# Kernel tuning notes

Measured on AMD Instinct MI355X. Metric: run time of the kernel, lower is better.

The kernel has to match this reference:

```python
import jax, jax.numpy as jnp
import numpy as np

N_HEADS = 32
N_KV_HEADS = 8
HEAD_DIM = 64
ROPE_THETA = 10000.0
NEG_INF = -1e9


def apply_rope(t, offset=0):
    # t: [B, H, L, hd]; half-split (rotate-half) RoPE convention
    B, H, L, hd = t.shape
    pos = jnp.arange(offset, offset + L, dtype=jnp.float32)            # [L]
    inv_freq = 1.0 / (ROPE_THETA ** (jnp.arange(0, hd, 2, dtype=jnp.float32) / hd))  # [hd/2]
    ang = pos[:, None] * inv_freq[None, :]                              # [L, hd/2]
    cos = jnp.cos(ang).astype(t.dtype)
    sin = jnp.sin(ang).astype(t.dtype)
    t1, t2 = jnp.split(t, 2, axis=-1)                                   # each [B,H,L,hd/2]
    return jnp.concatenate([t1 * cos - t2 * sin, t1 * sin + t2 * cos], axis=-1)


def setup_inputs() -> dict:
    key = jax.random.key(0)
    ks = jax.random.split(key, 6)
    B, L, D = 1, 2048, 2048
    x = jax.random.normal(ks[0], (B, L, D), dtype=jnp.float32)
    attn_scale = jnp.ones((1,), dtype=jnp.float32)
    # causal additive mask: 0 on/below diagonal, -1e9 above
    mask = jnp.where(jnp.tril(jnp.ones((L, L), dtype=bool)), 0.0, NEG_INF).astype(jnp.float32)
    s = 0.02
    Wq = jax.random.normal(ks[1], (N_HEADS * HEAD_DIM, D), dtype=jnp.float32) * s
    Wk = jax.random.normal(ks[2], (N_KV_HEADS * HEAD_DIM, D), dtype=jnp.float32) * s
    Wv = jax.random.normal(ks[3], (N_KV_HEADS * HEAD_DIM, D), dtype=jnp.float32) * s
    Wo = jax.random.normal(ks[4], (D, N_HEADS * HEAD_DIM), dtype=jnp.float32) * s
    return {"x": x, "attn_scale": attn_scale, "mask": mask,
            "Wq": Wq, "Wk": Wk, "Wv": Wv, "Wo": Wo}


def reference(x, attn_scale, mask, Wq, Wk, Wv, Wo):
    B, L, D = x.shape
    scale = HEAD_DIM ** -0.5
    # projections (nn.Linear: y = x @ W.T)
    q = (x @ Wq.T).reshape(B, L, N_HEADS, HEAD_DIM).transpose(0, 2, 1, 3)     # [B,H,L,hd]
    k = (x @ Wk.T).reshape(B, L, N_KV_HEADS, HEAD_DIM).transpose(0, 2, 1, 3)  # [B,Hk,L,hd]
    v = (x @ Wv.T).reshape(B, L, N_KV_HEADS, HEAD_DIM).transpose(0, 2, 1, 3)
    q = apply_rope(q)
    k = apply_rope(k)
    q = q * attn_scale  # elementwise attn_scale applied to queries
    # GQA: repeat kv heads
    rep = N_HEADS // N_KV_HEADS
    k = jnp.repeat(k, rep, axis=1)
    v = jnp.repeat(v, rep, axis=1)
    scores = jnp.einsum('bhld,bhmd->bhlm', q, k) * scale + mask
    probs = jax.nn.softmax(scores, axis=-1)
    out = jnp.einsum('bhlm,bhmd->bhld', probs, v)          # [B,H,L,hd]
    out = out.transpose(0, 2, 1, 3).reshape(B, L, N_HEADS * HEAD_DIM)
    return out @ Wo.T
```

## Files before the change

### kernel.cpp

```cpp
#include <hip/hip_runtime.h>
#include <stdint.h>

typedef short bf16x8 __attribute__((ext_vector_type(8)));
typedef float f32x4 __attribute__((ext_vector_type(4)));

__device__ __forceinline__ unsigned short f2bf(float f) {
  uint32_t u = __float_as_uint(f);
  u = (u + 0x7FFFu + ((u >> 16) & 1u)) >> 16;
  return (unsigned short)u;
}
__device__ __forceinline__ float bf2f(unsigned short h) {
  return __uint_as_float(((uint32_t)h) << 16);
}

__device__ __forceinline__ void gload16(const void* g, void* lds) {
  const __attribute__((address_space(1))) char* gp =
      (const __attribute__((address_space(1))) char*)(uintptr_t)g;
  __attribute__((address_space(3))) char* sp =
      (__attribute__((address_space(3))) char*)(uint32_t)(uintptr_t)lds;
  __builtin_amdgcn_global_load_lds(gp, sp, 16, 0, 0);
}

__global__ void k_cvt_all(const float* __restrict__ x, const float* __restrict__ Wq,
                          const float* __restrict__ Wk, const float* __restrict__ Wv,
                          const float* __restrict__ Wo, unsigned short* __restrict__ xb,
                          unsigned short* __restrict__ Wcat, unsigned short* __restrict__ Wob) {
  int b = blockIdx.x;
  const float* src;
  unsigned short* dst;
  int off;
  if (b < 4096)       { src = x;  dst = xb;                  off = b; }
  else if (b < 8192)  { src = Wq; dst = Wcat;                off = b - 4096; }
  else if (b < 9216)  { src = Wk; dst = Wcat + 2048 * 2048;  off = b - 8192; }
  else if (b < 10240) { src = Wv; dst = Wcat + 2560 * 2048;  off = b - 9216; }
  else                { src = Wo; dst = Wob;                  off = b - 10240; }
  int i = off * 256 + threadIdx.x;
  float4 v = ((const float4*)src)[i];
  ushort4 o;
  o.x = f2bf(v.x); o.y = f2bf(v.y); o.z = f2bf(v.z); o.w = f2bf(v.w);
  ((ushort4*)dst)[i] = o;
}

template <int OUTF32>
__global__ __launch_bounds__(256) void k_gemm(const unsigned short* __restrict__ A,
                                              const unsigned short* __restrict__ B,
                                              void* __restrict__ Cout,
                                              int M, int N, int K) {
  __shared__ unsigned short As[2][128 * 64];
  __shared__ unsigned short Bs[2][128 * 64];
  const int tid = threadIdx.x;
  const int w = tid >> 6, lane = tid & 63;
  const int g = lane >> 4, cl = lane & 15;
  const int nTn = N >> 7;
  const int per = gridDim.x >> 3;
  const int bid = (blockIdx.x & 7) * per + (blockIdx.x >> 3);
  const int tm = bid / nTn, tn = bid % nTn;
  const int m0 = tm << 7, n0 = tn << 7;
  const int wm = (w >> 1) << 6, wn = (w & 1) << 6;
  f32x4 acc[4][4] = {};

  auto stage = [&](int kt, int b) {
#pragma unroll
    for (int it = 0; it < 8; ++it) {
      int cc = tid + it * 256;
      int half = cc >> 10;
      int c3 = cc & 1023;
      int row = c3 >> 3, kb = (c3 & 7) << 4;
      const unsigned short* base = half ? (B + (size_t)(n0 + row) * K + kt)
                                        : (A + (size_t)(m0 + row) * K + kt);
      const char* src = (const char*)base + (kb ^ ((row & 7) << 4));
      char* dstl = (char*)(half ? Bs[b] : As[b]) + c3 * 16;
      gload16(src, dstl);
    }
  };

  stage(0, 0);
  asm volatile("s_waitcnt vmcnt(0)" ::: "memory");
  __syncthreads();
  int buf = 0;

  for (int kt = 0; kt < K; kt += 64) {
    if (kt + 64 < K) stage(kt + 64, buf ^ 1);
#pragma unroll
    for (int ks = 0; ks < 2; ++ks) {
      bf16x8 af[4], bfr[4];
#pragma unroll
      for (int i = 0; i < 4; ++i) {
        int row = wm + i * 16 + cl;
        int kb = ((g << 4) + (ks << 6)) ^ ((row & 7) << 4);
        af[i] = *(const bf16x8*)((const char*)As[buf] + row * 128 + kb);
      }
#pragma unroll
      for (int j = 0; j < 4; ++j) {
        int row = wn + j * 16 + cl;
        int kb = ((g << 4) + (ks << 6)) ^ ((row & 7) << 4);
        bfr[j] = *(const bf16x8*)((const char*)Bs[buf] + row * 128 + kb);
      }
#pragma unroll
      for (int i = 0; i < 4; ++i)
#pragma unroll
        for (int j = 0; j < 4; ++j)
          acc[i][j] = __builtin_amdgcn_mfma_f32_16x16x32_bf16(af[i], bfr[j], acc[i][j], 0, 0, 0);
    }
    asm volatile("s_waitcnt vmcnt(0)" ::: "memory");
    __syncthreads();
    buf ^= 1;
  }
#pragma unroll
  for (int i = 0; i < 4; ++i)
#pragma unroll
    for (int j = 0; j < 4; ++j)
#pragma unroll
      for (int r = 0; r < 4; ++r) {
        int row = m0 + wm + i * 16 + (g << 2) + r;
        int col = n0 + wn + j * 16 + cl;
        float v = acc[i][j][r];
        if (OUTF32)
          ((float*)Cout)[(size_t)row * N + col] = v;
        else
          ((unsigned short*)Cout)[(size_t)row * N + col] = f2bf(v);
      }
}

__global__ void k_ropevt(unsigned short* __restrict__ qkv, const float* __restrict__ scale_p,
                         unsigned short* __restrict__ vt) {
  __shared__ unsigned short tl[64][80];
  if (blockIdx.x < 2560) {
    int idx = blockIdx.x * 256 + threadIdx.x;
    int l = idx / 320;
    int u = idx - l * 320;
    int h = u >> 3;
    int i4 = (u & 7) << 2;
    int colbase = (h < 32) ? (h << 6) : (2048 + ((h - 32) << 6));
    unsigned short* p = qkv + (size_t)l * 3072 + colbase + i4;
    float sc = (h < 32) ? (scale_p[0] * 0.125f * 1.4426950408889634f) : 1.0f;
    ushort4 a = *(const ushort4*)p;
    ushort4 b = *(const ushort4*)(p + 32);
    unsigned short av[4] = {a.x, a.y, a.z, a.w};
    unsigned short bv[4] = {b.x, b.y, b.z, b.w};
    unsigned short r1[4], r2[4];
#pragma unroll
    for (int j = 0; j < 4; ++j) {
      int i = i4 + j;
      float invf = __expf(-(float)i * 0.2878231366242557f);
      float ang = (float)l * invf;
      float cs = cosf(ang), sn = sinf(ang);
      float x1 = bf2f(av[j]), x2 = bf2f(bv[j]);
      r1[j] = f2bf((x1 * cs - x2 * sn) * sc);
      r2[j] = f2bf((x1 * sn + x2 * cs) * sc);
    }
    ushort4 oa = {r1[0], r1[1], r1[2], r1[3]};
    ushort4 ob = {r2[0], r2[1], r2[2], r2[3]};
    *(ushort4*)p = oa;
    *(ushort4*)(p + 32) = ob;
  } else {
    const int tid = threadIdx.x;
    const int bb = blockIdx.x - 2560;
    const int hk = bb >> 5, lt = bb & 31;
    const int l0 = lt << 6;
#pragma unroll
    for (int it = 0; it < 2; ++it) {
      int cc = tid + it * 256;
      int lr = cc >> 3, d0 = (cc & 7) << 3;
      uint4 v = *(const uint4*)(qkv + (size_t)(l0 + lr) * 3072 + 2560 + hk * 64 + d0);
      *(uint4*)&tl[lr][d0] = v;
    }
    __syncthreads();
#pragma unroll
    for (int it = 0; it < 2; ++it) {
      int cc = tid + it * 256;
      int dr = cc >> 3, le = (cc & 7) << 3;
      unsigned short tmp[8] __attribute__((aligned(16)));
#pragma unroll
      for (int j = 0; j < 8; ++j) tmp[j] = tl[le + j][dr];
      *(uint4*)(vt + (size_t)(hk * 64 + dr) * 2048 + l0 + le) = *(const uint4*)tmp;
    }
  }
}

__global__ __launch_bounds__(256) void k_attn(const unsigned short* __restrict__ qkv,
                                              const unsigned short* __restrict__ vt,
                                              unsigned short* __restrict__ ao) {
  __shared__ unsigned short Ks[2][64 * 64];
  __shared__ unsigned short Vs[3][64 * 64];
  __shared__ unsigned short Ps[4 * 16 * 64];
  const int tid = threadIdx.x;
  const int w = tid >> 6, lane = tid & 63;
  const int g = lane >> 4, cl = lane & 15;
  const int h = blockIdx.x & 31;
  const int qb = 31 - (blockIdx.x >> 5);
  const int q0 = qb << 6;
  const int hk = h >> 2;
  const int qg = q0 + w * 16 + cl;

  const unsigned short* qptr = qkv + (size_t)qg * 3072 + h * 64 + g * 8;
  bf16x8 qf0 = *(const bf16x8*)qptr;
  bf16x8 qf1 = *(const bf16x8*)(qptr + 32);

  float m_run = -3e38f, l_run = 0.0f;
  f32x4 acc[4] = {};

  const unsigned short* kbase = qkv + 2048 + hk * 64;
  const unsigned short* vbase = vt + (size_t)hk * 64 * 2048;
  char* myP = (char*)Ps + w * 2048;

  auto stageK = [&](int ck, int b) {
    const int kv0 = ck << 6;
#pragma unroll
    for (int it = 0; it < 2; ++it) {
      int cc = tid + it * 256;
      int row = cc >> 3, kb = (cc & 7) << 4;
      const char* src = (const char*)(kbase + (size_t)(kv0 + row) * 3072) + (kb ^ ((row & 7) << 4));
      gload16(src, (char*)Ks[b] + cc * 16);
    }
  };
  auto stageV = [&](int ck, int b) {
    const int kv0 = ck << 6;
#pragma unroll
    for (int it = 0; it < 2; ++it) {
      int cc = tid + it * 256;
      int row = cc >> 3, kb = (cc & 7) << 4;
      const char* src = (const char*)(vbase + (size_t)row * 2048 + kv0) + (kb ^ ((row & 7) << 4));
      gload16(src, (char*)Vs[b] + cc * 16);
    }
  };

  stageK(0, 0); stageV(0, 0);
  if (qb >= 1) { stageK(1, 1); stageV(1, 1); }
  asm volatile("s_waitcnt vmcnt(0)" ::: "memory");
  __syncthreads();

  float svP[4][4];
  {
    const char* Kc = (const char*)Ks[0];
    __builtin_amdgcn_s_setprio(1);
#pragma unroll
    for (int t = 0; t < 4; ++t) {
      f32x4 st = {};
#pragma unroll
      for (int ks = 0; ks < 2; ++ks) {
        int row = t * 16 + cl;
        int kb = ((g << 4) + (ks << 6)) ^ ((row & 7) << 4);
        bf16x8 kf = *(const bf16x8*)(Kc + row * 128 + kb);
        st = __builtin_amdgcn_mfma_f32_16x16x32_bf16(kf, ks ? qf1 : qf0, st, 0, 0, 0);
      }
#pragma unroll
      for (int r = 0; r < 4; ++r) svP[t][r] = st[r];
    }
    __builtin_amdgcn_s_setprio(0);
  }
  __syncthreads();

  for (int i = 0; i <= qb; ++i) {
    const bool deep = (i + 2 <= qb);
    if (deep) stageK(i + 2, (i + 2) & 1);

    float svN[4][4];
    if (i < qb) {
      const char* Kc = (const char*)Ks[(i + 1) & 1];
      __builtin_amdgcn_s_setprio(1);
#pragma unroll
      for (int t = 0; t < 4; ++t) {
        f32x4 st = {};
#pragma unroll
        for (int ks = 0; ks < 2; ++ks) {
          int row = t * 16 + cl;
          int kb = ((g << 4) + (ks << 6)) ^ ((row & 7) << 4);
          bf16x8 kf = *(const bf16x8*)(Kc + row * 128 + kb);
          st = __builtin_amdgcn_mfma_f32_16x16x32_bf16(kf, ks ? qf1 : qf0, st, 0, 0, 0);
        }
#pragma unroll
        for (int r = 0; r < 4; ++r) svN[t][r] = st[r];
      }
      __builtin_amdgcn_s_setprio(0);
    }

    if (deep) stageV(i + 2, (i + 2) % 3);

    if (i == qb) {
      const int kv0 = i << 6;
#pragma unroll
      for (int t = 0; t < 4; ++t)
#pragma unroll
        for (int r = 0; r < 4; ++r) {
          int kvg = kv0 + t * 16 + (g << 2) + r;
          if (kvg > qg) svP[t][r] = -1e9f;
        }
    }
    float pm[4];
#pragma unroll
    for (int t = 0; t < 4; ++t)
      pm[t] = fmaxf(fmaxf(svP[t][0], svP[t][1]), fmaxf(svP[t][2], svP[t][3]));
    float pmax = fmaxf(fmaxf(pm[0], pm[1]), fmaxf(pm[2], pm[3]));
    pmax = fmaxf(pmax, __shfl_xor(pmax, 16));
    pmax = fmaxf(pmax, __shfl_xor(pmax, 32));
    if (!__all(pmax - m_run <= 8.0f)) {
      float m_new = fmaxf(m_run, pmax);
      float fac = __builtin_exp2f(m_run - m_new);
      float fr[4];
#pragma unroll
      for (int r = 0; r < 4; ++r) fr[r] = __shfl(fac, (g << 2) + r);
#pragma unroll
      for (int t = 0; t < 4; ++t) {
        acc[t][0] *= fr[0]; acc[t][1] *= fr[1]; acc[t][2] *= fr[2]; acc[t][3] *= fr[3];
      }
      l_run *= fac;
      m_run = m_new;
    }
    float ps[4];
#pragma unroll
    for (int t = 0; t < 4; ++t) {
      float e0 = __builtin_exp2f(svP[t][0] - m_run);
      float e1 = __builtin_exp2f(svP[t][1] - m_run);
      float e2 = __builtin_exp2f(svP[t][2] - m_run);
      float e3 = __builtin_exp2f(svP[t][3] - m_run);
      ps[t] = (e0 + e1) + (e2 + e3);
      uint32_t d0, d1;
      asm("v_cvt_pk_bf16_f32 %0, %1, %2" : "=v"(d0) : "v"(e0), "v"(e1));
      asm("v_cvt_pk_bf16_f32 %0, %1, %2" : "=v"(d1) : "v"(e2), "v"(e3));
      uint2 dd; dd.x = d0; dd.y = d1;
      int kb = ((t << 5) + (g << 3)) ^ ((cl & 7) << 4);
      *(uint2*)(myP + cl * 128 + kb) = dd;
    }
    float psum = (ps[0] + ps[1]) + (ps[2] + ps[3]);
    psum += __shfl_xor(psum, 16);
    psum += __shfl_xor(psum, 32);
    l_run += psum;

    {
      const char* Vc = (const char*)Vs[i % 3];
      __builtin_amdgcn_s_setprio(1);
#pragma unroll
      for (int ks = 0; ks < 2; ++ks) {
        int kbp = ((g << 4) + (ks << 6)) ^ ((cl & 7) << 4);
        bf16x8 pf = *(const bf16x8*)(myP + cl * 128 + kbp);
#pragma unroll
        for (int t = 0; t < 4; ++t) {
          int row = t * 16 + cl;
          int kbv = ((g << 4) + (ks << 6)) ^ ((row & 7) << 4);
          bf16x8 vf = *(const bf16x8*)(Vc + row * 128 + kbv);
          acc[t] = __builtin_amdgcn_mfma_f32_16x16x32_bf16(pf, vf, acc[t], 0, 0, 0);
        }
      }
      __builtin_amdgcn_s_setprio(0);
    }

    if (i < qb) {
      if (deep)
        asm volatile("s_waitcnt vmcnt(2)" ::: "memory");
      else
        asm volatile("s_waitcnt vmcnt(0)" ::: "memory");
      __syncthreads();
#pragma unroll
      for (int t = 0; t < 4; ++t)
#pragma unroll
        for (int r = 0; r < 4; ++r) svP[t][r] = svN[t][r];
    }
  }

  float li[4];
#pragma unroll
  for (int r = 0; r < 4; ++r) li[r] = 1.0f / __shfl(l_run, (g << 2) + r);
#pragma unroll
  for (int t = 0; t < 4; ++t)
#pragma unroll
    for (int r = 0; r < 4; ++r) {
      int row = q0 + w * 16 + (g << 2) + r;
      int col = h * 64 + t * 16 + cl;
      ao[(size_t)row * 2048 + col] = f2bf(acc[t][r] * li[r]);
    }
}

extern "C" void kernel_launch(void* const* d_in, const int* in_sizes, int n_in,
                              void* d_out, int out_size, void* d_ws, size_t ws_size,
                              hipStream_t stream) {
  (void)in_sizes; (void)n_in; (void)out_size; (void)ws_size;
  const float* x  = (const float*)d_in[0];
  const float* sc = (const float*)d_in[1];
  const float* Wq = (const float*)d_in[3];
  const float* Wk = (const float*)d_in[4];
  const float* Wv = (const float*)d_in[5];
  const float* Wo = (const float*)d_in[6];
  float* out = (float*)d_out;
  char* ws = (char*)d_ws;
  unsigned short* xb   = (unsigned short*)(ws);
  unsigned short* Wcat = (unsigned short*)(ws + 8388608);
  unsigned short* Wob  = (unsigned short*)(ws + 20971520);
  unsigned short* QKV  = (unsigned short*)(ws + 29360128);
  unsigned short* VT   = (unsigned short*)(ws + 41943040);
  unsigned short* AO   = (unsigned short*)(ws + 44040192);

  k_cvt_all<<<14336, 256, 0, stream>>>(x, Wq, Wk, Wv, Wo, xb, Wcat, Wob);
  k_gemm<0><<<384, 256, 0, stream>>>(xb, Wcat, QKV, 2048, 3072, 2048);
  k_ropevt<<<2816, 256, 0, stream>>>(QKV, sc, VT);
  k_attn<<<1024, 256, 0, stream>>>(QKV, VT, AO);
  k_gemm<1><<<256, 256, 0, stream>>>(AO, Wob, out, 2048, 2048, 2048);
}
```

Before: 128.9 us.

## Split attention into single-wave blocks with V loaded directly to registers

The attention kernel changes from 256-thread blocks, where four waves share staged K and V tiles, to 64-thread single-wave blocks, each handling 16 query rows, with four times as many blocks. V fragments are now read straight from global memory into registers instead of through a triple-buffered LDS stage. K is single-buffered in LDS with a prefetch of the next chunk, and the block barriers are removed. This gives up K/V reuse across four waves and the deep software pipeline in exchange for no barriers and more scheduling freedom. Global K/V traffic roughly quadruples, and memory latency is less well hidden.

```diff
diff --git a/kernel.cpp b/kernel.cpp
--- a/kernel.cpp
+++ b/kernel.cpp
@@ -178,61 +178,58 @@
   }
 }
 
-__global__ __launch_bounds__(256) void k_attn(const unsigned short* __restrict__ qkv,
-                                              const unsigned short* __restrict__ vt,
-                                              unsigned short* __restrict__ ao) {
-  __shared__ unsigned short Ks[2][64 * 64];
-  __shared__ unsigned short Vs[3][64 * 64];
-  __shared__ unsigned short Ps[4 * 16 * 64];
-  const int tid = threadIdx.x;
-  const int w = tid >> 6, lane = tid & 63;
+__global__ __launch_bounds__(64, 4) void k_attn(const unsigned short* __restrict__ qkv,
+                                                const unsigned short* __restrict__ vt,
+                                                unsigned short* __restrict__ ao) {
+  __shared__ unsigned short Ks[64 * 64];
+  __shared__ unsigned short Ps[16 * 64];
+  const int lane = threadIdx.x;
   const int g = lane >> 4, cl = lane & 15;
   const int h = blockIdx.x & 31;
-  const int qb = 31 - (blockIdx.x >> 5);
-  const int q0 = qb << 6;
+  const int rest = blockIdx.x >> 5;
+  const int qb = 31 - (rest >> 2);
+  const int quarter = rest & 3;
+  const int q0 = (qb << 6) + (quarter << 4);
   const int hk = h >> 2;
-  const int qg = q0 + w * 16 + cl;
+  const int qg = q0 + cl;
 
   const unsigned short* qptr = qkv + (size_t)qg * 3072 + h * 64 + g * 8;
+  const unsigned short* kbase = qkv + 2048 + hk * 64;
+  const unsigned short* vbase = vt + (size_t)hk * 64 * 2048;
+  char* myP = (char*)Ps;
+
+  auto stageK = [&](int ck) {
+    const int kv0 = ck << 6;
+#pragma unroll
+    for (int it = 0; it < 8; ++it) {
+      int cc = lane + it * 64;
+      int row = cc >> 3, kb = (cc & 7) << 4;
+      const char* src = (const char*)(kbase + (size_t)(kv0 + row) * 3072) + (kb ^ ((row & 7) << 4));
+      gload16(src, (char*)Ks + cc * 16);
+    }
+  };
+
+  stageK(0);
   bf16x8 qf0 = *(const bf16x8*)qptr;
   bf16x8 qf1 = *(const bf16x8*)(qptr + 32);
+  asm volatile("s_waitcnt vmcnt(0)" ::: "memory");
 
   float m_run = -3e38f, l_run = 0.0f;
   f32x4 acc[4] = {};
 
-  const unsigned short* kbase = qkv + 2048 + hk * 64;
-  const unsigned short* vbase = vt + (size_t)hk * 64 * 2048;
-  char* myP = (char*)Ps + w * 2048;
-
-  auto stageK = [&](int ck, int b) {
-    const int kv0 = ck << 6;
-#pragma unroll
-    for (int it = 0; it < 2; ++it) {
-      int cc = tid + it * 256;
-      int row = cc >> 3, kb = (cc & 7) << 4;
-      const char* src = (const char*)(kbase + (size_t)(kv0 + row) * 3072) + (kb ^ ((row & 7) << 4));
-      gload16(src, (char*)Ks[b] + cc * 16);
-    }
-  };
-  auto stageV = [&](int ck, int b) {
-    const int kv0 = ck << 6;
-#pragma unroll
-    for (int it = 0; it < 2; ++it) {
-      int cc = tid + it * 256;
-      int row = cc >> 3, kb = (cc & 7) << 4;
-      const char* src = (const char*)(vbase + (size_t)row * 2048 + kv0) + (kb ^ ((row & 7) << 4));
-      gload16(src, (char*)Vs[b] + cc * 16);
-    }
-  };
-
-  stageK(0, 0); stageV(0, 0);
-  if (qb >= 1) { stageK(1, 1); stageV(1, 1); }
-  asm volatile("s_waitcnt vmcnt(0)" ::: "memory");
-  __syncthreads();
-
-  float svP[4][4];
-  {
-    const char* Kc = (const char*)Ks[0];
+  for (int i = 0; i <= qb; ++i) {
+    const int kv0 = i << 6;
+
+    bf16x8 vfr[2][4];
+#pragma unroll
+    for (int ks = 0; ks < 2; ++ks)
+#pragma unroll
+      for (int t = 0; t < 4; ++t)
+        vfr[ks][t] = *(const bf16x8*)(vbase + (size_t)(t * 16 + cl) * 2048 + kv0 + ks * 32 + g * 8);
+
+    asm volatile("s_waitcnt vmcnt(8)" ::: "memory");
+
+    float svP[4][4];
     __builtin_amdgcn_s_setprio(1);
 #pragma unroll
     for (int t = 0; t < 4; ++t) {
@@ -241,44 +238,18 @@
       for (int ks = 0; ks < 2; ++ks) {
         int row = t * 16 + cl;
         int kb = ((g << 4) + (ks << 6)) ^ ((row & 7) << 4);
-        bf16x8 kf = *(const bf16x8*)(Kc + row * 128 + kb);
+        bf16x8 kf = *(const bf16x8*)((const char*)Ks + row * 128 + kb);
         st = __builtin_amdgcn_mfma_f32_16x16x32_bf16(kf, ks ? qf1 : qf0, st, 0, 0, 0);
       }
 #pragma unroll
       for (int r = 0; r < 4; ++r) svP[t][r] = st[r];
     }
     __builtin_amdgcn_s_setprio(0);
-  }
-  __syncthreads();
-
-  for (int i = 0; i <= qb; ++i) {
-    const bool deep = (i + 2 <= qb);
-    if (deep) stageK(i + 2, (i + 2) & 1);
-
-    float svN[4][4];
-    if (i < qb) {
-      const char* Kc = (const char*)Ks[(i + 1) & 1];
-      __builtin_amdgcn_s_setprio(1);
-#pragma unroll
-      for (int t = 0; t < 4; ++t) {
-        f32x4 st = {};
-#pragma unroll
-        for (int ks = 0; ks < 2; ++ks) {
-          int row = t * 16 + cl;
-          int kb = ((g << 4) + (ks << 6)) ^ ((row & 7) << 4);
-          bf16x8 kf = *(const bf16x8*)(Kc + row * 128 + kb);
-          st = __builtin_amdgcn_mfma_f32_16x16x32_bf16(kf, ks ? qf1 : qf0, st, 0, 0, 0);
-        }
-#pragma unroll
-        for (int r = 0; r < 4; ++r) svN[t][r] = st[r];
-      }
-      __builtin_amdgcn_s_setprio(0);
-    }
-
-    if (deep) stageV(i + 2, (i + 2) % 3);
+
+    asm volatile("s_waitcnt lgkmcnt(0)" ::: "memory");
+    if (i < qb) stageK(i + 1);
 
     if (i == qb) {
-      const int kv0 = i << 6;
 #pragma unroll
       for (int t = 0; t < 4; ++t)
 #pragma unroll
@@ -327,35 +298,16 @@
     psum += __shfl_xor(psum, 32);
     l_run += psum;
 
-    {
-      const char* Vc = (const char*)Vs[i % 3];
-      __builtin_amdgcn_s_setprio(1);
-#pragma unroll
-      for (int ks = 0; ks < 2; ++ks) {
-        int kbp = ((g << 4) + (ks << 6)) ^ ((cl & 7) << 4);
-        bf16x8 pf = *(const bf16x8*)(myP + cl * 128 + kbp);
-#pragma unroll
-        for (int t = 0; t < 4; ++t) {
-          int row = t * 16 + cl;
-          int kbv = ((g << 4) + (ks << 6)) ^ ((row & 7) << 4);
-          bf16x8 vf = *(const bf16x8*)(Vc + row * 128 + kbv);
-          acc[t] = __builtin_amdgcn_mfma_f32_16x16x32_bf16(pf, vf, acc[t], 0, 0, 0);
-        }
-      }
-      __builtin_amdgcn_s_setprio(0);
-    }
-
-    if (i < qb) {
-      if (deep)
-        asm volatile("s_waitcnt vmcnt(2)" ::: "memory");
-      else
-        asm volatile("s_waitcnt vmcnt(0)" ::: "memory");
-      __syncthreads();
+    __builtin_amdgcn_s_setprio(1);
+#pragma unroll
+    for (int ks = 0; ks < 2; ++ks) {
+      int kbp = ((g << 4) + (ks << 6)) ^ ((cl & 7) << 4);
+      bf16x8 pf = *(const bf16x8*)(myP + cl * 128 + kbp);
 #pragma unroll
       for (int t = 0; t < 4; ++t)
-#pragma unroll
-        for (int r = 0; r < 4; ++r) svP[t][r] = svN[t][r];
-    }
+        acc[t] = __builtin_amdgcn_mfma_f32_16x16x32_bf16(pf, vfr[ks][t], acc[t], 0, 0, 0);
+    }
+    __builtin_amdgcn_s_setprio(0);
   }
 
   float li[4];
@@ -365,7 +317,7 @@
   for (int t = 0; t < 4; ++t)
 #pragma unroll
     for (int r = 0; r < 4; ++r) {
-      int row = q0 + w * 16 + (g << 2) + r;
+      int row = q0 + (g << 2) + r;
       int col = h * 64 + t * 16 + cl;
       ao[(size_t)row * 2048 + col] = f2bf(acc[t][r] * li[r]);
     }
@@ -393,6 +345,6 @@
   k_cvt_all<<<14336, 256, 0, stream>>>(x, Wq, Wk, Wv, Wo, xb, Wcat, Wob);
   k_gemm<0><<<384, 256, 0, stream>>>(xb, Wcat, QKV, 2048, 3072, 2048);
   k_ropevt<<<2816, 256, 0, stream>>>(QKV, sc, VT);
-  k_attn<<<1024, 256, 0, stream>>>(QKV, VT, AO);
+  k_attn<<<4096, 64, 0, stream>>>(QKV, VT, AO);
   k_gemm<1><<<256, 256, 0, stream>>>(AO, Wob, out, 2048, 2048, 2048);
 }
```

Result: slower. 218.4 us (+69.4%).

## Fuse RoPE and scaling into QKV GEMM epilogue; simplify attention V buffering

Applied to the files above, without the earlier changes.

RoPE rotation and the query scale move into the QKV projection GEMM epilogue, operating on fp32 accumulators before the bf16 store. This removes a separate read-modify-write pass over Q and K and leaves a small kernel that only transposes V. The attention kernel also goes from triple- to double-buffered V staging, with V prefetched one tile ahead and a full vmcnt(0) wait each iteration. That cuts LDS use but may expose more load latency. Rotating before bf16 rounding also slightly changes numerics.

```diff
diff --git a/kernel.cpp b/kernel.cpp
--- a/kernel.cpp
+++ b/kernel.cpp
@@ -41,11 +41,12 @@
   ((ushort4*)dst)[i] = o;
 }
 
-template <int OUTF32>
+template <int OUTF32, int ROPE>
 __global__ __launch_bounds__(256) void k_gemm(const unsigned short* __restrict__ A,
                                               const unsigned short* __restrict__ B,
                                               void* __restrict__ Cout,
-                                              int M, int N, int K) {
+                                              int M, int N, int K,
+                                              const float* __restrict__ scale_p) {
   __shared__ unsigned short As[2][128 * 64];
   __shared__ unsigned short Bs[2][128 * 64];
   const int tid = threadIdx.x;
@@ -106,6 +107,31 @@
     __syncthreads();
     buf ^= 1;
   }
+
+  if (ROPE && n0 < 2560) {
+    float s0v = scale_p[0] * 0.125f * 1.4426950408889634f;
+    float sc = (n0 < 2048) ? s0v : 1.0f;
+    float invf[2];
+#pragma unroll
+    for (int j = 0; j < 2; ++j)
+      invf[j] = __expf(-(float)(j * 16 + cl) * 0.2878231366242557f);
+#pragma unroll
+    for (int i = 0; i < 4; ++i)
+#pragma unroll
+      for (int r = 0; r < 4; ++r) {
+        float pos = (float)(m0 + wm + i * 16 + (g << 2) + r);
+#pragma unroll
+        for (int j = 0; j < 2; ++j) {
+          float ang = pos * invf[j];
+          float sn, cs;
+          __sincosf(ang, &sn, &cs);
+          float t1 = acc[i][j][r], t2 = acc[i][j + 2][r];
+          acc[i][j][r] = (t1 * cs - t2 * sn) * sc;
+          acc[i][j + 2][r] = (t1 * sn + t2 * cs) * sc;
+        }
+      }
+  }
+
 #pragma unroll
   for (int i = 0; i < 4; ++i)
 #pragma unroll
@@ -122,59 +148,27 @@
       }
 }
 
-__global__ void k_ropevt(unsigned short* __restrict__ qkv, const float* __restrict__ scale_p,
-                         unsigned short* __restrict__ vt) {
+__global__ void k_vt(const unsigned short* __restrict__ qkv, unsigned short* __restrict__ vt) {
   __shared__ unsigned short tl[64][80];
-  if (blockIdx.x < 2560) {
-    int idx = blockIdx.x * 256 + threadIdx.x;
-    int l = idx / 320;
-    int u = idx - l * 320;
-    int h = u >> 3;
-    int i4 = (u & 7) << 2;
-    int colbase = (h < 32) ? (h << 6) : (2048 + ((h - 32) << 6));
-    unsigned short* p = qkv + (size_t)l * 3072 + colbase + i4;
-    float sc = (h < 32) ? (scale_p[0] * 0.125f * 1.4426950408889634f) : 1.0f;
-    ushort4 a = *(const ushort4*)p;
-    ushort4 b = *(const ushort4*)(p + 32);
-    unsigned short av[4] = {a.x, a.y, a.z, a.w};
-    unsigned short bv[4] = {b.x, b.y, b.z, b.w};
-    unsigned short r1[4], r2[4];
-#pragma unroll
-    for (int j = 0; j < 4; ++j) {
-      int i = i4 + j;
-      float invf = __expf(-(float)i * 0.2878231366242557f);
-      float ang = (float)l * invf;
-      float cs = cosf(ang), sn = sinf(ang);
-      float x1 = bf2f(av[j]), x2 = bf2f(bv[j]);
-      r1[j] = f2bf((x1 * cs - x2 * sn) * sc);
-      r2[j] = f2bf((x1 * sn + x2 * cs) * sc);
-    }
-    ushort4 oa = {r1[0], r1[1], r1[2], r1[3]};
-    ushort4 ob = {r2[0], r2[1], r2[2], r2[3]};
-    *(ushort4*)p = oa;
-    *(ushort4*)(p + 32) = ob;
-  } else {
-    const int tid = threadIdx.x;
-    const int bb = blockIdx.x - 2560;
-    const int hk = bb >> 5, lt = bb & 31;
-    const int l0 = lt << 6;
-#pragma unroll
-    for (int it = 0; it < 2; ++it) {
-      int cc = tid + it * 256;
-      int lr = cc >> 3, d0 = (cc & 7) << 3;
-      uint4 v = *(const uint4*)(qkv + (size_t)(l0 + lr) * 3072 + 2560 + hk * 64 + d0);
-      *(uint4*)&tl[lr][d0] = v;
-    }
-    __syncthreads();
-#pragma unroll
-    for (int it = 0; it < 2; ++it) {
-      int cc = tid + it * 256;
-      int dr = cc >> 3, le = (cc & 7) << 3;
-      unsigned short tmp[8] __attribute__((aligned(16)));
-#pragma unroll
-      for (int j = 0; j < 8; ++j) tmp[j] = tl[le + j][dr];
-      *(uint4*)(vt + (size_t)(hk * 64 + dr) * 2048 + l0 + le) = *(const uint4*)tmp;
-    }
+  const int tid = threadIdx.x;
+  const int hk = blockIdx.x >> 5, lt = blockIdx.x & 31;
+  const int l0 = lt << 6;
+#pragma unroll
+  for (int it = 0; it < 2; ++it) {
+    int cc = tid + it * 256;
+    int lr = cc >> 3, d0 = (cc & 7) << 3;
+    uint4 v = *(const uint4*)(qkv + (size_t)(l0 + lr) * 3072 + 2560 + hk * 64 + d0);
+    *(uint4*)&tl[lr][d0] = v;
+  }
+  __syncthreads();
+#pragma unroll
+  for (int it = 0; it < 2; ++it) {
+    int cc = tid + it * 256;
+    int dr = cc >> 3, le = (cc & 7) << 3;
+    unsigned short tmp[8] __attribute__((aligned(16)));
+#pragma unroll
+    for (int j = 0; j < 8; ++j) tmp[j] = tl[le + j][dr];
+    *(uint4*)(vt + (size_t)(hk * 64 + dr) * 2048 + l0 + le) = *(const uint4*)tmp;
   }
 }
 
@@ -182,7 +176,7 @@
                                               const unsigned short* __restrict__ vt,
                                               unsigned short* __restrict__ ao) {
   __shared__ unsigned short Ks[2][64 * 64];
-  __shared__ unsigned short Vs[3][64 * 64];
+  __shared__ unsigned short Vs[2][64 * 64];
   __shared__ unsigned short Ps[4 * 16 * 64];
   const int tid = threadIdx.x;
   const int w = tid >> 6, lane = tid & 63;
@@ -226,7 +220,7 @@
   };
 
   stageK(0, 0); stageV(0, 0);
-  if (qb >= 1) { stageK(1, 1); stageV(1, 1); }
+  if (qb >= 1) stageK(1, 1);
   asm volatile("s_waitcnt vmcnt(0)" ::: "memory");
   __syncthreads();
 
@@ -252,8 +246,8 @@
   __syncthreads();
 
   for (int i = 0; i <= qb; ++i) {
-    const bool deep = (i + 2 <= qb);
-    if (deep) stageK(i + 2, (i + 2) & 1);
+    if (i + 2 <= qb) stageK(i + 2, i & 1);
+    if (i + 1 <= qb) stageV(i + 1, (i + 1) & 1);
 
     float svN[4][4];
     if (i < qb) {
@@ -274,8 +268,6 @@
       }
       __builtin_amdgcn_s_setprio(0);
     }
-
-    if (deep) stageV(i + 2, (i + 2) % 3);
 
     if (i == qb) {
       const int kv0 = i << 6;
@@ -328,7 +320,7 @@
     l_run += psum;
 
     {
-      const char* Vc = (const char*)Vs[i % 3];
+      const char* Vc = (const char*)Vs[i & 1];
       __builtin_amdgcn_s_setprio(1);
 #pragma unroll
       for (int ks = 0; ks < 2; ++ks) {
@@ -346,10 +338,7 @@
     }
 
     if (i < qb) {
-      if (deep)
-        asm volatile("s_waitcnt vmcnt(2)" ::: "memory");
-      else
-        asm volatile("s_waitcnt vmcnt(0)" ::: "memory");
+      asm volatile("s_waitcnt vmcnt(0)" ::: "memory");
       __syncthreads();
 #pragma unroll
       for (int t = 0; t < 4; ++t)
@@ -391,8 +380,8 @@
   unsigned short* AO   = (unsigned short*)(ws + 44040192);
 
   k_cvt_all<<<14336, 256, 0, stream>>>(x, Wq, Wk, Wv, Wo, xb, Wcat, Wob);
-  k_gemm<0><<<384, 256, 0, stream>>>(xb, Wcat, QKV, 2048, 3072, 2048);
-  k_ropevt<<<2816, 256, 0, stream>>>(QKV, sc, VT);
+  k_gemm<0, 1><<<384, 256, 0, stream>>>(xb, Wcat, QKV, 2048, 3072, 2048, sc);
+  k_vt<<<256, 256, 0, stream>>>(QKV, VT);
   k_attn<<<1024, 256, 0, stream>>>(QKV, VT, AO);
-  k_gemm<1><<<256, 256, 0, stream>>>(AO, Wob, out, 2048, 2048, 2048);
-}
+  k_gemm<1, 0><<<256, 256, 0, stream>>>(AO, Wob, out, 2048, 2048, 2048, nullptr);
+}
```

New measurement: 126.0 us. 2.3% less time.
